# Optimization experiments

Hardware: AMD Instinct MI355X
Metric: run time of the kernel (lower is better)

Reference implementation:

```python
import jax, jax.numpy as jnp
import numpy as np

N = 4096
SPECIES = 100
FEA = 64        # atom_emb_dim
NBR_FEA = 64    # num gaussians
MAX_NBRS = 12
LN_EPS = 1e-5

# GaussianSmearing constants: linspace(0, 8, 64)
_OFFSET = jnp.linspace(0.0, 8.0, NBR_FEA)
_COEFF = -0.5 / float(8.0 / (NBR_FEA - 1)) ** 2


def _uniform(key, shape, fan_in):
    s = 1.0 / np.sqrt(fan_in)
    return jax.random.uniform(key, shape, minval=-s, maxval=s, dtype=jnp.float32)


def setup_inputs() -> dict:
    key = jax.random.key(0)
    ks = jax.random.split(key, 20)
    lat_pred = jnp.eye(3, dtype=jnp.float32) * 8.0 + 0.2 * jax.random.normal(ks[0], (3, 3), dtype=jnp.float32)
    fracs_pred = jax.random.uniform(ks[1], (N, 3), dtype=jnp.float32)
    species_logits = jax.random.normal(ks[2], (N, SPECIES), dtype=jnp.float32)
    occ_logits = jax.random.normal(ks[3], (N,), dtype=jnp.float32)
    # params
    emb_w = _uniform(ks[4], (SPECIES, FEA), SPECIES)
    emb_b = _uniform(ks[5], (FEA,), SPECIES)
    in1 = 2 * FEA + NBR_FEA  # 192
    w1 = _uniform(ks[6], (in1, 2 * FEA), in1)
    b1 = _uniform(ks[7], (2 * FEA,), in1)
    g1 = jnp.ones((2 * FEA,), jnp.float32)
    be1 = jnp.zeros((2 * FEA,), jnp.float32)
    w2 = _uniform(ks[8], (in1, 2 * FEA), in1)
    b2 = _uniform(ks[9], (2 * FEA,), in1)
    g2 = jnp.ones((2 * FEA,), jnp.float32)
    be2 = jnp.zeros((2 * FEA,), jnp.float32)
    fc_w = _uniform(ks[10], (FEA, 1), FEA)
    fc_b = _uniform(ks[11], (1,), FEA)
    return dict(lat_pred=lat_pred, fracs_pred=fracs_pred, species_logits=species_logits,
                occ_logits=occ_logits, emb_w=emb_w, emb_b=emb_b,
                w1=w1, b1=b1, g1=g1, be1=be1, w2=w2, b2=b2, g2=g2, be2=be2,
                fc_w=fc_w, fc_b=fc_b)


def _layernorm(x, g, b):
    m = jnp.mean(x, axis=-1, keepdims=True)
    v = jnp.var(x, axis=-1, keepdims=True)
    return (x - m) * jax.lax.rsqrt(v + LN_EPS) * g + b


def _cgcnn_layer(atom, nbr_atom, nbr_fea, w, b, g, be):
    # atom: [N,F]; nbr_atom: [N,M,F]; nbr_fea: [N,M,K]
    n, m = nbr_atom.shape[:2]
    atom_exp = jnp.broadcast_to(atom[:, None, :], (n, m, atom.shape[-1]))
    total = jnp.concatenate([atom_exp, nbr_atom, nbr_fea], axis=2)  # [N,M,2F+K]
    z = _layernorm(total @ w + b, g, be)                            # [N,M,2F]
    nbr_filter, nbr_core = jnp.split(z, 2, axis=2)
    nbr_sumed = jnp.sum(jax.nn.sigmoid(nbr_filter) * jax.nn.softplus(nbr_core), axis=1)
    return jax.nn.softplus(atom + nbr_sumed)


def reference(lat_pred, fracs_pred, species_logits, occ_logits,
              emb_w, emb_b, w1, b1, g1, be1, w2, b2, g2, be2, fc_w, fc_b):
    species_probs = jax.nn.softmax(species_logits, axis=-1)
    atom_fea = species_probs @ emb_w + emb_b                         # [N,F]
    diff = fracs_pred[:, None, :] - fracs_pred[None, :, :]           # [N,N,3]
    diff = diff - jnp.round(diff)                                    # min-image
    cart = diff @ lat_pred                                           # [N,N,3]
    dist = jnp.linalg.norm(cart, axis=-1)                            # [N,N]
    dist = dist + jnp.eye(dist.shape[0], dtype=dist.dtype) * 100.0
    k = min(MAX_NBRS, dist.shape[1] - 1)
    neg_d, nbr_idx = jax.lax.top_k(-dist, k)                         # smallest k
    nbr_dist = -neg_d                                                # [N,k]
    nbr_fea = jnp.exp(_COEFF * (nbr_dist[..., None] - _OFFSET) ** 2) # [N,k,K]
    nbr_atom_fea = atom_fea[nbr_idx]                                 # [N,k,F]
    atom_fea = _cgcnn_layer(atom_fea, nbr_atom_fea, nbr_fea, w1, b1, g1, be1)
    atom_fea = _cgcnn_layer(atom_fea, nbr_atom_fea, nbr_fea, w2, b2, g2, be2)
    occ_probs = jax.nn.sigmoid(occ_logits)[:, None]                  # [N,1]
    graph_fea = jnp.sum(atom_fea * occ_probs, axis=0) / (jnp.sum(occ_probs) + 1e-6)
    return graph_fea @ fc_w + fc_b                                   # [1]
```

## Files before the change

### kernel.cpp

```cpp
#include <hip/hip_runtime.h>
#include <math.h>

#define N_ATOMS 4096
#define SPECIES 100
#define FEA 64
#define M_NBR 12

typedef unsigned short u16;
typedef __attribute__((ext_vector_type(8))) _Float16 f16x8;
typedef __attribute__((ext_vector_type(4))) float f32x4;

constexpr float LN_EPS = 1e-5f;
constexpr float GAUSS_COEFF = -31.0078125f;
constexpr float D2_INF = 3.4e38f;

__device__ __forceinline__ float sigmoidf_(float x){
    return __fdividef(1.0f, 1.0f + __expf(-x));
}
__device__ __forceinline__ float softplusf_(float x){
    return fmaxf(x, 0.0f) + __logf(1.0f + __expf(-fabsf(x)));
}
__device__ __forceinline__ u16 f16bits(_Float16 h){ return *(u16*)&h; }

__global__ __launch_bounds__(256) void k_setup(const float* __restrict__ fracs,
        const float* __restrict__ w1, const float* __restrict__ w2,
        const float* __restrict__ logits, const float* __restrict__ emb_w,
        const float* __restrict__ emb_b,
        float* __restrict__ fx, float* __restrict__ fy, float* __restrict__ fz,
        u16* __restrict__ wpk, float* __restrict__ atom0, u16* __restrict__ a0f){
    __shared__ float sE[4][SPECIES];
    int b = blockIdx.x, t = threadIdx.x;
    if (b < 192){
        int gid = b * 256 + t;
        int layer = gid / 24576;
        int e = gid % 24576;
        int k = e >> 7, n = e & 127;
        float x = (layer ? w2 : w1)[e];
        int mat = layer * 3 + (k >> 6);
        int kk = k & 63;
        int ch = kk >> 5, lg2 = (kk >> 3) & 3, i = kk & 7;
        int nt = n >> 4, lr2 = n & 15;
        wpk[mat * 8192 + ((ch * 8 + nt) * 64 + (lg2 * 16 + lr2)) * 8 + i] = f16bits((_Float16)x);
    } else if (b < 208){
        int j = (b - 192) * 256 + t;
        fx[j] = fracs[j*3+0];
        fy[j] = fracs[j*3+1];
        fz[j] = fracs[j*3+2];
    } else {
        int grp = t >> 6, f = t & 63;
        int a = (b - 208) * 4 + grp;
        const float* lg = logits + (long)a * SPECIES;
        float l0 = lg[f];
        float l1 = (f + 64 < SPECIES) ? lg[f + 64] : -1e30f;
        float mx = fmaxf(l0, l1);
        #pragma unroll
        for (int off = 32; off; off >>= 1) mx = fmaxf(mx, __shfl_xor(mx, off));
        float e0 = __expf(l0 - mx);
        float e1 = (f + 64 < SPECIES) ? __expf(l1 - mx) : 0.0f;
        sE[grp][f] = e0;
        if (f + 64 < SPECIES) sE[grp][64 + f] = e1;
        float sm = e0 + e1;
        #pragma unroll
        for (int off = 32; off; off >>= 1) sm += __shfl_xor(sm, off);
        __syncthreads();
        float acc = 0.0f;
        for (int s = 0; s < SPECIES; ++s) acc += sE[grp][s] * emb_w[s * FEA + f];
        float v = acc / sm + emb_b[f];
        atom0[(long)a * FEA + f] = v;
        a0f[a * FEA + f] = f16bits((_Float16)v);
    }
}

__global__ __launch_bounds__(256) void k_topk(const float* __restrict__ fx,
        const float* __restrict__ fy, const float* __restrict__ fz,
        const float* __restrict__ lat, int* __restrict__ nbr_idx,
        float* __restrict__ nbr_dist){
    __shared__ int   hist[256];
    __shared__ int   cnt;
    __shared__ float sThr;
    __shared__ float candD[256];
    __shared__ int   candI[256];
    int i = blockIdx.x, tid = threadIdx.x;
    hist[tid] = 0;
    if (tid == 0) cnt = 0;
    __syncthreads();
    float l00=lat[0],l01=lat[1],l02=lat[2];
    float l10=lat[3],l11=lat[4],l12=lat[5];
    float l20=lat[6],l21=lat[7],l22=lat[8];
    float xi = fx[i], yi = fy[i], zi = fz[i];
    float d2r[16];
    #pragma unroll
    for (int k = 0; k < 16; ++k){
        int j = tid + k * 256;
        float dx = xi - fx[j];
        float dy = yi - fy[j];
        float dz = zi - fz[j];
        dx -= rintf(dx); dy -= rintf(dy); dz -= rintf(dz);
        float cx = dx*l00 + dy*l10 + dz*l20;
        float cy = dx*l01 + dy*l11 + dz*l21;
        float cz = dx*l02 + dy*l12 + dz*l22;
        float d2 = cx*cx + cy*cy + cz*cz;
        if (j == i) d2 = D2_INF;
        d2r[k] = d2;
        if (d2 < 4.0f) atomicAdd(&hist[(int)(d2 * 64.0f)], 1);
    }
    __syncthreads();
    if (tid < 64){
        int s0 = hist[4*tid] + hist[4*tid+1] + hist[4*tid+2] + hist[4*tid+3];
        int sc = s0;
        #pragma unroll
        for (int off = 1; off < 64; off <<= 1){
            int o = __shfl_up(sc, off);
            if (tid >= off) sc += o;
        }
        unsigned long long mball = __ballot(sc >= M_NBR);
        if (mball == 0ULL){
            if (tid == 0) sThr = 1e30f;
        } else {
            int gbin = __ffsll(mball) - 1;
            if (tid == gbin){
                int c = sc - s0;
                float th = 4.0f;
                #pragma unroll
                for (int b = 0; b < 4; ++b){
                    c += hist[4*gbin + b];
                    if (c >= M_NBR){ th = (float)(4*gbin + b + 1) * (1.0f/64.0f); break; }
                }
                sThr = th;
            }
        }
    }
    __syncthreads();
    float thr = sThr;
    #pragma unroll
    for (int k = 0; k < 16; ++k){
        if (d2r[k] < thr){
            int p = atomicAdd(&cnt, 1);
            if (p < 256){ candD[p] = d2r[k]; candI[p] = tid + k * 256; }
        }
    }
    __syncthreads();
    int n = cnt < 256 ? cnt : 256;
    for (int c = tid; c < n; c += 256){
        float dv = candD[c]; int iv = candI[c];
        int rank = 0;
        for (int s = 0; s < n; ++s){
            float ds_ = candD[s]; int is_ = candI[s];
            rank += (ds_ < dv || (ds_ == dv && is_ < iv)) ? 1 : 0;
        }
        if (rank < M_NBR){
            nbr_idx[i * M_NBR + rank]  = iv;
            nbr_dist[i * M_NBR + rank] = sqrtf(dv);
        }
    }
}

__global__ __launch_bounds__(192) void k_fused(
        const float* __restrict__ atom0F, const u16* __restrict__ a0f,
        const int* __restrict__ nbr_idx, const float* __restrict__ nbr_dist,
        const u16* __restrict__ wpk,
        const float* __restrict__ b1, const float* __restrict__ g1, const float* __restrict__ be1,
        const float* __restrict__ b2, const float* __restrict__ g2, const float* __restrict__ be2,
        float* __restrict__ outF)
{
    __shared__ float sS1[4][132];
    __shared__ float prod[48][68];
    __shared__ float sSF[4][64];
    __shared__ u16   sSH[4][64];
    __shared__ float sS2[4][132];

    const int t = threadIdx.x;
    const int w = t >> 6, l = t & 63;
    const int lg = l >> 4, lr = l & 15;
    const int blk = blockIdx.x;
    const int row = blk * 48 + w * 16 + lr;

    const int nid = nbr_idx[row];
    f16x8 nfr[2];
    nfr[0] = *(const f16x8*)(a0f + nid * 64 + lg * 8);
    nfr[1] = *(const f16x8*)(a0f + nid * 64 + 32 + lg * 8);

    f16x8 saf[2];
    if (w == 1){
        #pragma unroll
        for (int c = 0; c < 2; ++c)
            saf[c] = (lr < 4) ? *(const f16x8*)(a0f + (blk * 4 + lr) * 64 + c * 32 + lg * 8)
                              : (f16x8)0;
    }

    float g1v[8], be1v[8], g2v[8], be2v[8];
    #pragma unroll
    for (int nt = 0; nt < 8; ++nt){
        int c = nt * 16 + lr;
        g1v[nt] = g1[c]; be1v[nt] = be1[c];
        g2v[nt] = g2[c]; be2v[nt] = be2[c];
    }

    const float dist = nbr_dist[row];
    f16x8 ga[2];
    #pragma unroll
    for (int c = 0; c < 2; ++c)
        #pragma unroll
        for (int i = 0; i < 8; ++i){
            int k = c * 32 + lg * 8 + i;
            float dd = dist - (float)k * (8.0f / 63.0f);
            ga[c][i] = (_Float16)__expf(GAUSS_COEFF * dd * dd);
        }

    int aloc[4];
    #pragma unroll
    for (int rr = 0; rr < 4; ++rr)
        aloc[rr] = (w * 16 + lg * 4 + rr) / 12;

    const u16* ws1 = wpk;
    const u16* wn1 = wpk + 1 * 8192;
    const u16* wg1 = wpk + 2 * 8192;
    const u16* ws2 = wpk + 3 * 8192;
    const u16* wn2 = wpk + 4 * 8192;
    const u16* wg2 = wpk + 5 * 8192;

    if (w == 1){
        f32x4 a1[8];
        #pragma unroll
        for (int nt = 0; nt < 8; ++nt) a1[nt] = 0.0f;
        #pragma unroll
        for (int c = 0; c < 2; ++c)
            #pragma unroll
            for (int nt = 0; nt < 8; ++nt){
                const f16x8 b = *(const f16x8*)(ws1 + ((c * 8 + nt) * 64 + l) * 8);
                a1[nt] = __builtin_amdgcn_mfma_f32_16x16x32_f16(saf[c], b, a1[nt], 0, 0, 0);
            }
        if (lg == 0){
            #pragma unroll
            for (int nt = 0; nt < 8; ++nt)
                #pragma unroll
                for (int rr = 0; rr < 4; ++rr)
                    sS1[rr][nt * 16 + lr] = a1[nt][rr] + b1[nt * 16 + lr];
        }
    }

    f32x4 acc[8], acc2[8];
    #pragma unroll
    for (int nt = 0; nt < 8; ++nt){ acc[nt] = 0.0f; acc2[nt] = 0.0f; }
    #pragma unroll
    for (int c = 0; c < 2; ++c)
        #pragma unroll
        for (int nt = 0; nt < 8; ++nt){
            const f16x8 bn1 = *(const f16x8*)(wn1 + ((c * 8 + nt) * 64 + l) * 8);
            acc[nt]  = __builtin_amdgcn_mfma_f32_16x16x32_f16(nfr[c], bn1, acc[nt], 0, 0, 0);
            const f16x8 bg1 = *(const f16x8*)(wg1 + ((c * 8 + nt) * 64 + l) * 8);
            acc[nt]  = __builtin_amdgcn_mfma_f32_16x16x32_f16(ga[c],  bg1, acc[nt], 0, 0, 0);
            const f16x8 bn2 = *(const f16x8*)(wn2 + ((c * 8 + nt) * 64 + l) * 8);
            acc2[nt] = __builtin_amdgcn_mfma_f32_16x16x32_f16(nfr[c], bn2, acc2[nt], 0, 0, 0);
            const f16x8 bg2 = *(const f16x8*)(wg2 + ((c * 8 + nt) * 64 + l) * 8);
            acc2[nt] = __builtin_amdgcn_mfma_f32_16x16x32_f16(ga[c],  bg2, acc2[nt], 0, 0, 0);
        }
    __syncthreads();

    {
        float s[4] = {0,0,0,0}, q[4] = {0,0,0,0};
        #pragma unroll
        for (int nt = 0; nt < 8; ++nt)
            #pragma unroll
            for (int rr = 0; rr < 4; ++rr){
                float v = acc[nt][rr] + sS1[aloc[rr]][nt * 16 + lr];
                acc[nt][rr] = v;
                s[rr] += v; q[rr] += v * v;
            }
        #pragma unroll
        for (int rr = 0; rr < 4; ++rr){
            #pragma unroll
            for (int m = 1; m < 16; m <<= 1){
                s[rr] += __shfl_xor(s[rr], m);
                q[rr] += __shfl_xor(q[rr], m);
            }
        }
        #pragma unroll
        for (int rr = 0; rr < 4; ++rr){
            float mean = s[rr] * (1.0f / 128.0f);
            float var  = q[rr] * (1.0f / 128.0f) - mean * mean;
            float inv  = rsqrtf(var + LN_EPS);
            #pragma unroll
            for (int nt = 0; nt < 4; ++nt){
                float zf = (acc[nt][rr]     - mean) * inv * g1v[nt]     + be1v[nt];
                float zc = (acc[nt + 4][rr] - mean) * inv * g1v[nt + 4] + be1v[nt + 4];
                prod[w * 16 + lg * 4 + rr][nt * 16 + lr] = sigmoidf_(zf) * softplusf_(zc);
            }
        }
    }
    __syncthreads();

    #pragma unroll
    for (int rep = 0; rep < 2; ++rep){
        int item = t + rep * 192;
        if (item < 256){
            int a_ = item >> 6, c = item & 63;
            float sm = 0.0f;
            #pragma unroll
            for (int m = 0; m < 12; ++m) sm += prod[a_ * 12 + m][c];
            float o = softplusf_(atom0F[(long)(blk * 4 + a_) * 64 + c] + sm);
            sSF[a_][c] = o;
            sSH[a_][c] = f16bits((_Float16)o);
        }
    }
    __syncthreads();

    if (w == 0){
        f16x8 af[2];
        #pragma unroll
        for (int c = 0; c < 2; ++c)
            af[c] = (lr < 4) ? *(const f16x8*)(&sSH[lr][c * 32 + lg * 8]) : (f16x8)0;
        f32x4 a2[8];
        #pragma unroll
        for (int nt = 0; nt < 8; ++nt) a2[nt] = 0.0f;
        #pragma unroll
        for (int c = 0; c < 2; ++c)
            #pragma unroll
            for (int nt = 0; nt < 8; ++nt){
                const f16x8 b = *(const f16x8*)(ws2 + ((c * 8 + nt) * 64 + l) * 8);
                a2[nt] = __builtin_amdgcn_mfma_f32_16x16x32_f16(af[c], b, a2[nt], 0, 0, 0);
            }
        if (lg == 0){
            #pragma unroll
            for (int nt = 0; nt < 8; ++nt)
                #pragma unroll
                for (int rr = 0; rr < 4; ++rr)
                    sS2[rr][nt * 16 + lr] = a2[nt][rr] + b2[nt * 16 + lr];
        }
    }
    __syncthreads();

    {
        float s[4] = {0,0,0,0}, q[4] = {0,0,0,0};
        #pragma unroll
        for (int nt = 0; nt < 8; ++nt)
            #pragma unroll
            for (int rr = 0; rr < 4; ++rr){
                float v = acc2[nt][rr] + sS2[aloc[rr]][nt * 16 + lr];
                acc2[nt][rr] = v;
                s[rr] += v; q[rr] += v * v;
            }
        #pragma unroll
        for (int rr = 0; rr < 4; ++rr){
            #pragma unroll
            for (int m = 1; m < 16; m <<= 1){
                s[rr] += __shfl_xor(s[rr], m);
                q[rr] += __shfl_xor(q[rr], m);
            }
        }
        #pragma unroll
        for (int rr = 0; rr < 4; ++rr){
            float mean = s[rr] * (1.0f / 128.0f);
            float var  = q[rr] * (1.0f / 128.0f) - mean * mean;
            float inv  = rsqrtf(var + LN_EPS);
            #pragma unroll
            for (int nt = 0; nt < 4; ++nt){
                float zf = (acc2[nt][rr]     - mean) * inv * g2v[nt]     + be2v[nt];
                float zc = (acc2[nt + 4][rr] - mean) * inv * g2v[nt + 4] + be2v[nt + 4];
                prod[w * 16 + lg * 4 + rr][nt * 16 + lr] = sigmoidf_(zf) * softplusf_(zc);
            }
        }
    }
    __syncthreads();

    #pragma unroll
    for (int rep = 0; rep < 2; ++rep){
        int item = t + rep * 192;
        if (item < 256){
            int a_ = item >> 6, c = item & 63;
            float sm = 0.0f;
            #pragma unroll
            for (int m = 0; m < 12; ++m) sm += prod[a_ * 12 + m][c];
            outF[(long)(blk * 4 + a_) * 64 + c] = softplusf_(sSF[a_][c] + sm);
        }
    }
}

__global__ __launch_bounds__(256) void k_partial(const float* __restrict__ atom,
        const float* __restrict__ occ, float* __restrict__ partials){
    int b = blockIdx.x, tid = threadIdx.x;
    int f = tid & 63, sub = tid >> 6;
    __shared__ float sAcc[256];
    float acc = 0.0f;
    for (int it = 0; it < 16; ++it){
        int a = b * 64 + sub + it * 4;
        float p = sigmoidf_(occ[a]);
        acc += atom[(long)a * FEA + f] * p;
    }
    sAcc[tid] = acc;
    __syncthreads();
    if (tid < 64){
        float s = sAcc[f] + sAcc[64 + f] + sAcc[128 + f] + sAcc[192 + f];
        partials[b * 65 + f] = s;
        float po = sigmoidf_(occ[b * 64 + f]);
        #pragma unroll
        for (int off = 32; off; off >>= 1) po += __shfl_down(po, off);
        if (f == 0) partials[b * 65 + 64] = po;
    }
}

__global__ __launch_bounds__(64) void k_final(const float* __restrict__ partials,
        const float* __restrict__ fc_w, const float* __restrict__ fc_b,
        float* __restrict__ out){
    int f = threadIdx.x;
    float num = 0.0f;
    for (int p = 0; p < 64; ++p) num += partials[p * 65 + f];
    float occs = partials[f * 65 + 64];
    #pragma unroll
    for (int off = 32; off; off >>= 1) occs += __shfl_down(occs, off);
    occs = __shfl(occs, 0);
    float gf = num / (occs + 1e-6f);
    float v = gf * fc_w[f];
    #pragma unroll
    for (int off = 32; off; off >>= 1) v += __shfl_down(v, off);
    if (f == 0) out[0] = v + fc_b[0];
}

extern "C" void kernel_launch(void* const* d_in, const int* in_sizes, int n_in,
                              void* d_out, int out_size, void* d_ws, size_t ws_size,
                              hipStream_t stream) {
    const float* lat    = (const float*)d_in[0];
    const float* fracs  = (const float*)d_in[1];
    const float* slog   = (const float*)d_in[2];
    const float* occ    = (const float*)d_in[3];
    const float* emb_w  = (const float*)d_in[4];
    const float* emb_b  = (const float*)d_in[5];
    const float* w1     = (const float*)d_in[6];
    const float* b1     = (const float*)d_in[7];
    const float* g1     = (const float*)d_in[8];
    const float* be1    = (const float*)d_in[9];
    const float* w2     = (const float*)d_in[10];
    const float* b2     = (const float*)d_in[11];
    const float* g2     = (const float*)d_in[12];
    const float* be2    = (const float*)d_in[13];
    const float* fc_w   = (const float*)d_in[14];
    const float* fc_b   = (const float*)d_in[15];
    float* out = (float*)d_out;

    char* ws = (char*)d_ws;
    auto alloc = [&](size_t bytes) -> void* {
        void* p = (void*)ws;
        ws += (bytes + 255) & ~(size_t)255;
        return p;
    };
    int*   nbr_idx  = (int*)  alloc((size_t)N_ATOMS * M_NBR * 4);
    float* nbr_dist = (float*)alloc((size_t)N_ATOMS * M_NBR * 4);
    float* atom0    = (float*)alloc((size_t)N_ATOMS * FEA * 4);
    float* atom1    = (float*)alloc((size_t)N_ATOMS * FEA * 4);
    u16*   a0f      = (u16*)  alloc((size_t)N_ATOMS * FEA * 2);
    u16*   wpk      = (u16*)  alloc((size_t)6 * 8192 * 2);
    float* fxa      = (float*)alloc((size_t)N_ATOMS * 4);
    float* fya      = (float*)alloc((size_t)N_ATOMS * 4);
    float* fza      = (float*)alloc((size_t)N_ATOMS * 4);
    float* partials = (float*)alloc((size_t)64 * 65 * 4);

    k_setup  <<<208 + N_ATOMS / 4, 256, 0, stream>>>(fracs, w1, w2, slog, emb_w, emb_b,
                fxa, fya, fza, wpk, atom0, a0f);
    k_topk   <<<N_ATOMS, 256, 0, stream>>>(fxa, fya, fza, lat, nbr_idx, nbr_dist);
    k_fused  <<<N_ATOMS / 4, 192, 0, stream>>>(atom0, a0f, nbr_idx, nbr_dist,
                wpk, b1, g1, be1, b2, g2, be2, atom1);
    k_partial<<<64, 256, 0, stream>>>(atom1, occ, partials);
    k_final  <<<1, 64, 0, stream>>>(partials, fc_w, fc_b, out);
}
```

Before: 62.11 us.

## Compute self-projection redundantly per wave to drop block barriers and defer layer-2 GEMM

Every wave now computes the self-atom projection into its own shared-memory slot instead of one wave doing it for all, which removes two block-wide barriers. The layer-2 neighbour GEMM is moved after layer 1 so the acc2 registers are not live during layer 1, lowering register pressure. Residual atom features are prefetched early, and the aggregation loops are flattened. In exchange the small self-projection MFMAs run three times redundantly and shared memory grows.

Result: no change. 62.13 us (+0.0%).

```diff
diff --git a/kernel.cpp b/kernel.cpp
--- a/kernel.cpp
+++ b/kernel.cpp
@@ -163,11 +163,11 @@
         const float* __restrict__ b2, const float* __restrict__ g2, const float* __restrict__ be2,
         float* __restrict__ outF)
 {
-    __shared__ float sS1[4][132];
+    __shared__ float sS1w[3][4][132];
+    __shared__ float sS2w[3][4][132];
     __shared__ float prod[48][68];
     __shared__ float sSF[4][64];
     __shared__ u16   sSH[4][64];
-    __shared__ float sS2[4][132];
 
     const int t = threadIdx.x;
     const int w = t >> 6, l = t & 63;
@@ -181,19 +181,20 @@
     nfr[1] = *(const f16x8*)(a0f + nid * 64 + 32 + lg * 8);
 
     f16x8 saf[2];
-    if (w == 1){
-        #pragma unroll
-        for (int c = 0; c < 2; ++c)
-            saf[c] = (lr < 4) ? *(const f16x8*)(a0f + (blk * 4 + lr) * 64 + c * 32 + lg * 8)
-                              : (f16x8)0;
-    }
-
-    float g1v[8], be1v[8], g2v[8], be2v[8];
+    #pragma unroll
+    for (int c = 0; c < 2; ++c)
+        saf[c] = (lr < 4) ? *(const f16x8*)(a0f + (blk * 4 + lr) * 64 + c * 32 + lg * 8)
+                          : (f16x8)0;
+
+    const float* a0flat = atom0F + (long)blk * 256;
+    float res0 = a0flat[t];
+    float res1 = (t < 64) ? a0flat[192 + t] : 0.0f;
+
+    float g1v[8], be1v[8];
     #pragma unroll
     for (int nt = 0; nt < 8; ++nt){
         int c = nt * 16 + lr;
         g1v[nt] = g1[c]; be1v[nt] = be1[c];
-        g2v[nt] = g2[c]; be2v[nt] = be2[c];
     }
 
     const float dist = nbr_dist[row];
@@ -219,7 +220,7 @@
     const u16* wn2 = wpk + 4 * 8192;
     const u16* wg2 = wpk + 5 * 8192;
 
-    if (w == 1){
+    {
         f32x4 a1[8];
         #pragma unroll
         for (int nt = 0; nt < 8; ++nt) a1[nt] = 0.0f;
@@ -235,27 +236,22 @@
             for (int nt = 0; nt < 8; ++nt)
                 #pragma unroll
                 for (int rr = 0; rr < 4; ++rr)
-                    sS1[rr][nt * 16 + lr] = a1[nt][rr] + b1[nt * 16 + lr];
-        }
-    }
-
-    f32x4 acc[8], acc2[8];
-    #pragma unroll
-    for (int nt = 0; nt < 8; ++nt){ acc[nt] = 0.0f; acc2[nt] = 0.0f; }
+                    sS1w[w][rr][nt * 16 + lr] = a1[nt][rr] + b1[nt * 16 + lr];
+        }
+    }
+
+    f32x4 acc[8];
+    #pragma unroll
+    for (int nt = 0; nt < 8; ++nt) acc[nt] = 0.0f;
     #pragma unroll
     for (int c = 0; c < 2; ++c)
         #pragma unroll
         for (int nt = 0; nt < 8; ++nt){
-            const f16x8 bn1 = *(const f16x8*)(wn1 + ((c * 8 + nt) * 64 + l) * 8);
-            acc[nt]  = __builtin_amdgcn_mfma_f32_16x16x32_f16(nfr[c], bn1, acc[nt], 0, 0, 0);
-            const f16x8 bg1 = *(const f16x8*)(wg1 + ((c * 8 + nt) * 64 + l) * 8);
-            acc[nt]  = __builtin_amdgcn_mfma_f32_16x16x32_f16(ga[c],  bg1, acc[nt], 0, 0, 0);
-            const f16x8 bn2 = *(const f16x8*)(wn2 + ((c * 8 + nt) * 64 + l) * 8);
-            acc2[nt] = __builtin_amdgcn_mfma_f32_16x16x32_f16(nfr[c], bn2, acc2[nt], 0, 0, 0);
-            const f16x8 bg2 = *(const f16x8*)(wg2 + ((c * 8 + nt) * 64 + l) * 8);
-            acc2[nt] = __builtin_amdgcn_mfma_f32_16x16x32_f16(ga[c],  bg2, acc2[nt], 0, 0, 0);
-        }
-    __syncthreads();
+            const f16x8 bn = *(const f16x8*)(wn1 + ((c * 8 + nt) * 64 + l) * 8);
+            acc[nt] = __builtin_amdgcn_mfma_f32_16x16x32_f16(nfr[c], bn, acc[nt], 0, 0, 0);
+            const f16x8 bg = *(const f16x8*)(wg1 + ((c * 8 + nt) * 64 + l) * 8);
+            acc[nt] = __builtin_amdgcn_mfma_f32_16x16x32_f16(ga[c], bg, acc[nt], 0, 0, 0);
+        }
 
     {
         float s[4] = {0,0,0,0}, q[4] = {0,0,0,0};
@@ -263,7 +259,7 @@
         for (int nt = 0; nt < 8; ++nt)
             #pragma unroll
             for (int rr = 0; rr < 4; ++rr){
-                float v = acc[nt][rr] + sS1[aloc[rr]][nt * 16 + lr];
+                float v = acc[nt][rr] + sS1w[w][aloc[rr]][nt * 16 + lr];
                 acc[nt][rr] = v;
                 s[rr] += v; q[rr] += v * v;
             }
@@ -290,22 +286,33 @@
     }
     __syncthreads();
 
-    #pragma unroll
-    for (int rep = 0; rep < 2; ++rep){
-        int item = t + rep * 192;
-        if (item < 256){
-            int a_ = item >> 6, c = item & 63;
-            float sm = 0.0f;
-            #pragma unroll
-            for (int m = 0; m < 12; ++m) sm += prod[a_ * 12 + m][c];
-            float o = softplusf_(atom0F[(long)(blk * 4 + a_) * 64 + c] + sm);
-            sSF[a_][c] = o;
-            sSH[a_][c] = f16bits((_Float16)o);
-        }
-    }
-    __syncthreads();
-
-    if (w == 0){
+    {
+        int a_ = t >> 6, c = t & 63;
+        float sm = 0.0f;
+        #pragma unroll
+        for (int m = 0; m < 12; ++m) sm += prod[a_ * 12 + m][c];
+        float o = softplusf_(res0 + sm);
+        sSF[a_][c] = o;
+        sSH[a_][c] = f16bits((_Float16)o);
+        if (t < 64){
+            float sm2 = 0.0f;
+            #pragma unroll
+            for (int m = 0; m < 12; ++m) sm2 += prod[36 + m][c];
+            float o2 = softplusf_(res1 + sm2);
+            sSF[3][c] = o2;
+            sSH[3][c] = f16bits((_Float16)o2);
+        }
+    }
+    __syncthreads();
+
+    float g2v[8], be2v[8];
+    #pragma unroll
+    for (int nt = 0; nt < 8; ++nt){
+        int c = nt * 16 + lr;
+        g2v[nt] = g2[c]; be2v[nt] = be2[c];
+    }
+
+    {
         f16x8 af[2];
         #pragma unroll
         for (int c = 0; c < 2; ++c)
@@ -325,10 +332,22 @@
             for (int nt = 0; nt < 8; ++nt)
                 #pragma unroll
                 for (int rr = 0; rr < 4; ++rr)
-                    sS2[rr][nt * 16 + lr] = a2[nt][rr] + b2[nt * 16 + lr];
-        }
-    }
-    __syncthreads();
+                    sS2w[w][rr][nt * 16 + lr] = a2[nt][rr] + b2[nt * 16 + lr];
+        }
+    }
+
+    f32x4 acc2[8];
+    #pragma unroll
+    for (int nt = 0; nt < 8; ++nt) acc2[nt] = 0.0f;
+    #pragma unroll
+    for (int c = 0; c < 2; ++c)
+        #pragma unroll
+        for (int nt = 0; nt < 8; ++nt){
+            const f16x8 bn = *(const f16x8*)(wn2 + ((c * 8 + nt) * 64 + l) * 8);
+            acc2[nt] = __builtin_amdgcn_mfma_f32_16x16x32_f16(nfr[c], bn, acc2[nt], 0, 0, 0);
+            const f16x8 bg = *(const f16x8*)(wg2 + ((c * 8 + nt) * 64 + l) * 8);
+            acc2[nt] = __builtin_amdgcn_mfma_f32_16x16x32_f16(ga[c], bg, acc2[nt], 0, 0, 0);
+        }
 
     {
         float s[4] = {0,0,0,0}, q[4] = {0,0,0,0};
@@ -336,7 +355,7 @@
         for (int nt = 0; nt < 8; ++nt)
             #pragma unroll
             for (int rr = 0; rr < 4; ++rr){
-                float v = acc2[nt][rr] + sS2[aloc[rr]][nt * 16 + lr];
+                float v = acc2[nt][rr] + sS2w[w][aloc[rr]][nt * 16 + lr];
                 acc2[nt][rr] = v;
                 s[rr] += v; q[rr] += v * v;
             }
@@ -363,15 +382,17 @@
     }
     __syncthreads();
 
-    #pragma unroll
-    for (int rep = 0; rep < 2; ++rep){
-        int item = t + rep * 192;
-        if (item < 256){
-            int a_ = item >> 6, c = item & 63;
-            float sm = 0.0f;
-            #pragma unroll
-            for (int m = 0; m < 12; ++m) sm += prod[a_ * 12 + m][c];
-            outF[(long)(blk * 4 + a_) * 64 + c] = softplusf_(sSF[a_][c] + sm);
+    {
+        int a_ = t >> 6, c = t & 63;
+        float sm = 0.0f;
+        #pragma unroll
+        for (int m = 0; m < 12; ++m) sm += prod[a_ * 12 + m][c];
+        outF[(long)blk * 256 + t] = softplusf_(sSF[a_][c] + sm);
+        if (t < 64){
+            float sm2 = 0.0f;
+            #pragma unroll
+            for (int m = 0; m < 12; ++m) sm2 += prod[36 + m][c];
+            outF[(long)blk * 256 + 192 + t] = softplusf_(sSF[3][c] + sm2);
         }
     }
 }
```

## Restructure fused CGCNN kernel to one wavefront per atom

Applied to the files above, without the earlier changes.

Replaces the 3-wave, 4-atoms-per-block fused layer kernel with a single-wavefront kernel that handles one atom per block. The 12 neighbours are padded to 16 MFMA rows, the self-feature GEMM is folded into the same MFMA accumulation, and the neighbour sum is done with lane shuffles instead of shared-memory reductions. The goal is to drop most block barriers and shared-memory traffic and to launch 4096 small blocks for better latency hiding. In exchange, every block redundantly runs the self GEMM over 16 rows, 4 padded rows are wasted per tile, and each block reloads the full weight set, which raises L2 traffic.

After: 61.85 us. About the same (-0.4%).

```diff
diff --git a/kernel.cpp b/kernel.cpp
--- a/kernel.cpp
+++ b/kernel.cpp
@@ -155,7 +155,7 @@
     }
 }
 
-__global__ __launch_bounds__(192) void k_fused(
+__global__ __launch_bounds__(64, 4) void k_atom(
         const float* __restrict__ atom0F, const u16* __restrict__ a0f,
         const int* __restrict__ nbr_idx, const float* __restrict__ nbr_dist,
         const u16* __restrict__ wpk,
@@ -163,40 +163,26 @@
         const float* __restrict__ b2, const float* __restrict__ g2, const float* __restrict__ be2,
         float* __restrict__ outF)
 {
-    __shared__ float sS1[4][132];
-    __shared__ float prod[48][68];
-    __shared__ float sSF[4][64];
-    __shared__ u16   sSH[4][64];
-    __shared__ float sS2[4][132];
-
-    const int t = threadIdx.x;
-    const int w = t >> 6, l = t & 63;
+    __shared__ u16   sH[64];
+    __shared__ float sO[64];
+
+    const int a = blockIdx.x;
+    const int l = threadIdx.x;
     const int lg = l >> 4, lr = l & 15;
-    const int blk = blockIdx.x;
-    const int row = blk * 48 + w * 16 + lr;
-
-    const int nid = nbr_idx[row];
-    f16x8 nfr[2];
+
+    const int slot = (lr < 12) ? lr : 11;
+    const int nid  = nbr_idx[a * M_NBR + slot];
+    const float dist = nbr_dist[a * M_NBR + slot];
+    f16x8 nfr[2], saf[2];
     nfr[0] = *(const f16x8*)(a0f + nid * 64 + lg * 8);
     nfr[1] = *(const f16x8*)(a0f + nid * 64 + 32 + lg * 8);
-
-    f16x8 saf[2];
-    if (w == 1){
-        #pragma unroll
-        for (int c = 0; c < 2; ++c)
-            saf[c] = (lr < 4) ? *(const f16x8*)(a0f + (blk * 4 + lr) * 64 + c * 32 + lg * 8)
-                              : (f16x8)0;
-    }
-
-    float g1v[8], be1v[8], g2v[8], be2v[8];
-    #pragma unroll
-    for (int nt = 0; nt < 8; ++nt){
-        int c = nt * 16 + lr;
-        g1v[nt] = g1[c]; be1v[nt] = be1[c];
-        g2v[nt] = g2[c]; be2v[nt] = be2[c];
-    }
-
-    const float dist = nbr_dist[row];
+    saf[0] = *(const f16x8*)(a0f + a * 64 + lg * 8);
+    saf[1] = *(const f16x8*)(a0f + a * 64 + 32 + lg * 8);
+    float resv[4];
+    #pragma unroll
+    for (int nt = 0; nt < 4; ++nt)
+        resv[nt] = atom0F[(long)a * 64 + nt * 16 + lr];
+
     f16x8 ga[2];
     #pragma unroll
     for (int c = 0; c < 2; ++c)
@@ -207,66 +193,39 @@
             ga[c][i] = (_Float16)__expf(GAUSS_COEFF * dd * dd);
         }
 
-    int aloc[4];
-    #pragma unroll
-    for (int rr = 0; rr < 4; ++rr)
-        aloc[rr] = (w * 16 + lg * 4 + rr) / 12;
-
-    const u16* ws1 = wpk;
-    const u16* wn1 = wpk + 1 * 8192;
-    const u16* wg1 = wpk + 2 * 8192;
-    const u16* ws2 = wpk + 3 * 8192;
-    const u16* wn2 = wpk + 4 * 8192;
-    const u16* wg2 = wpk + 5 * 8192;
-
-    if (w == 1){
-        f32x4 a1[8];
-        #pragma unroll
-        for (int nt = 0; nt < 8; ++nt) a1[nt] = 0.0f;
+    #pragma unroll 1
+    for (int layer = 0; layer < 2; ++layer){
+        const u16* wb = wpk + layer * 3 * 8192;
+        const float* bb  = layer ? b2  : b1;
+        const float* gg  = layer ? g2  : g1;
+        const float* bee = layer ? be2 : be1;
+
+        f32x4 acc[8];
+        #pragma unroll
+        for (int nt = 0; nt < 8; ++nt) acc[nt] = 0.0f;
         #pragma unroll
         for (int c = 0; c < 2; ++c)
             #pragma unroll
             for (int nt = 0; nt < 8; ++nt){
-                const f16x8 b = *(const f16x8*)(ws1 + ((c * 8 + nt) * 64 + l) * 8);
-                a1[nt] = __builtin_amdgcn_mfma_f32_16x16x32_f16(saf[c], b, a1[nt], 0, 0, 0);
-            }
-        if (lg == 0){
-            #pragma unroll
-            for (int nt = 0; nt < 8; ++nt)
-                #pragma unroll
-                for (int rr = 0; rr < 4; ++rr)
-                    sS1[rr][nt * 16 + lr] = a1[nt][rr] + b1[nt * 16 + lr];
-        }
-    }
-
-    f32x4 acc[8], acc2[8];
-    #pragma unroll
-    for (int nt = 0; nt < 8; ++nt){ acc[nt] = 0.0f; acc2[nt] = 0.0f; }
-    #pragma unroll
-    for (int c = 0; c < 2; ++c)
+                const f16x8 bS = *(const f16x8*)(wb +          ((c * 8 + nt) * 64 + l) * 8);
+                const f16x8 bN = *(const f16x8*)(wb +  8192 + ((c * 8 + nt) * 64 + l) * 8);
+                const f16x8 bG = *(const f16x8*)(wb + 16384 + ((c * 8 + nt) * 64 + l) * 8);
+                acc[nt] = __builtin_amdgcn_mfma_f32_16x16x32_f16(saf[c], bS, acc[nt], 0, 0, 0);
+                acc[nt] = __builtin_amdgcn_mfma_f32_16x16x32_f16(nfr[c], bN, acc[nt], 0, 0, 0);
+                acc[nt] = __builtin_amdgcn_mfma_f32_16x16x32_f16(ga[c],  bG, acc[nt], 0, 0, 0);
+            }
+
+        float s[4] = {0,0,0,0}, q[4] = {0,0,0,0};
         #pragma unroll
         for (int nt = 0; nt < 8; ++nt){
-            const f16x8 bn1 = *(const f16x8*)(wn1 + ((c * 8 + nt) * 64 + l) * 8);
-            acc[nt]  = __builtin_amdgcn_mfma_f32_16x16x32_f16(nfr[c], bn1, acc[nt], 0, 0, 0);
-            const f16x8 bg1 = *(const f16x8*)(wg1 + ((c * 8 + nt) * 64 + l) * 8);
-            acc[nt]  = __builtin_amdgcn_mfma_f32_16x16x32_f16(ga[c],  bg1, acc[nt], 0, 0, 0);
-            const f16x8 bn2 = *(const f16x8*)(wn2 + ((c * 8 + nt) * 64 + l) * 8);
-            acc2[nt] = __builtin_amdgcn_mfma_f32_16x16x32_f16(nfr[c], bn2, acc2[nt], 0, 0, 0);
-            const f16x8 bg2 = *(const f16x8*)(wg2 + ((c * 8 + nt) * 64 + l) * 8);
-            acc2[nt] = __builtin_amdgcn_mfma_f32_16x16x32_f16(ga[c],  bg2, acc2[nt], 0, 0, 0);
-        }
-    __syncthreads();
-
-    {
-        float s[4] = {0,0,0,0}, q[4] = {0,0,0,0};
-        #pragma unroll
-        for (int nt = 0; nt < 8; ++nt)
+            float bv = bb[nt * 16 + lr];
             #pragma unroll
             for (int rr = 0; rr < 4; ++rr){
-                float v = acc[nt][rr] + sS1[aloc[rr]][nt * 16 + lr];
+                float v = acc[nt][rr] + bv;
                 acc[nt][rr] = v;
                 s[rr] += v; q[rr] += v * v;
             }
+        }
         #pragma unroll
         for (int rr = 0; rr < 4; ++rr){
             #pragma unroll
@@ -275,103 +234,47 @@
                 q[rr] += __shfl_xor(q[rr], m);
             }
         }
-        #pragma unroll
-        for (int rr = 0; rr < 4; ++rr){
-            float mean = s[rr] * (1.0f / 128.0f);
-            float var  = q[rr] * (1.0f / 128.0f) - mean * mean;
-            float inv  = rsqrtf(var + LN_EPS);
-            #pragma unroll
-            for (int nt = 0; nt < 4; ++nt){
-                float zf = (acc[nt][rr]     - mean) * inv * g1v[nt]     + be1v[nt];
-                float zc = (acc[nt + 4][rr] - mean) * inv * g1v[nt + 4] + be1v[nt + 4];
-                prod[w * 16 + lg * 4 + rr][nt * 16 + lr] = sigmoidf_(zf) * softplusf_(zc);
-            }
-        }
-    }
-    __syncthreads();
-
-    #pragma unroll
-    for (int rep = 0; rep < 2; ++rep){
-        int item = t + rep * 192;
-        if (item < 256){
-            int a_ = item >> 6, c = item & 63;
-            float sm = 0.0f;
-            #pragma unroll
-            for (int m = 0; m < 12; ++m) sm += prod[a_ * 12 + m][c];
-            float o = softplusf_(atom0F[(long)(blk * 4 + a_) * 64 + c] + sm);
-            sSF[a_][c] = o;
-            sSH[a_][c] = f16bits((_Float16)o);
-        }
-    }
-    __syncthreads();
-
-    if (w == 0){
-        f16x8 af[2];
-        #pragma unroll
-        for (int c = 0; c < 2; ++c)
-            af[c] = (lr < 4) ? *(const f16x8*)(&sSH[lr][c * 32 + lg * 8]) : (f16x8)0;
-        f32x4 a2[8];
-        #pragma unroll
-        for (int nt = 0; nt < 8; ++nt) a2[nt] = 0.0f;
-        #pragma unroll
-        for (int c = 0; c < 2; ++c)
-            #pragma unroll
-            for (int nt = 0; nt < 8; ++nt){
-                const f16x8 b = *(const f16x8*)(ws2 + ((c * 8 + nt) * 64 + l) * 8);
-                a2[nt] = __builtin_amdgcn_mfma_f32_16x16x32_f16(af[c], b, a2[nt], 0, 0, 0);
-            }
-        if (lg == 0){
-            #pragma unroll
-            for (int nt = 0; nt < 8; ++nt)
-                #pragma unroll
-                for (int rr = 0; rr < 4; ++rr)
-                    sS2[rr][nt * 16 + lr] = a2[nt][rr] + b2[nt * 16 + lr];
-        }
-    }
-    __syncthreads();
-
-    {
-        float s[4] = {0,0,0,0}, q[4] = {0,0,0,0};
-        #pragma unroll
-        for (int nt = 0; nt < 8; ++nt)
+        float nsum[4];
+        #pragma unroll
+        for (int nt = 0; nt < 4; ++nt){
+            float gf = gg[nt * 16 + lr],      bef = bee[nt * 16 + lr];
+            float gc = gg[64 + nt * 16 + lr], bec = bee[64 + nt * 16 + lr];
+            float part = 0.0f;
             #pragma unroll
             for (int rr = 0; rr < 4; ++rr){
-                float v = acc2[nt][rr] + sS2[aloc[rr]][nt * 16 + lr];
-                acc2[nt][rr] = v;
-                s[rr] += v; q[rr] += v * v;
-            }
-        #pragma unroll
-        for (int rr = 0; rr < 4; ++rr){
-            #pragma unroll
-            for (int m = 1; m < 16; m <<= 1){
-                s[rr] += __shfl_xor(s[rr], m);
-                q[rr] += __shfl_xor(q[rr], m);
-            }
-        }
-        #pragma unroll
-        for (int rr = 0; rr < 4; ++rr){
-            float mean = s[rr] * (1.0f / 128.0f);
-            float var  = q[rr] * (1.0f / 128.0f) - mean * mean;
-            float inv  = rsqrtf(var + LN_EPS);
-            #pragma unroll
-            for (int nt = 0; nt < 4; ++nt){
-                float zf = (acc2[nt][rr]     - mean) * inv * g2v[nt]     + be2v[nt];
-                float zc = (acc2[nt + 4][rr] - mean) * inv * g2v[nt + 4] + be2v[nt + 4];
-                prod[w * 16 + lg * 4 + rr][nt * 16 + lr] = sigmoidf_(zf) * softplusf_(zc);
-            }
-        }
-    }
-    __syncthreads();
-
-    #pragma unroll
-    for (int rep = 0; rep < 2; ++rep){
-        int item = t + rep * 192;
-        if (item < 256){
-            int a_ = item >> 6, c = item & 63;
-            float sm = 0.0f;
-            #pragma unroll
-            for (int m = 0; m < 12; ++m) sm += prod[a_ * 12 + m][c];
-            outF[(long)(blk * 4 + a_) * 64 + c] = softplusf_(sSF[a_][c] + sm);
+                float mean = s[rr] * (1.0f / 128.0f);
+                float var  = q[rr] * (1.0f / 128.0f) - mean * mean;
+                float inv  = rsqrtf(var + LN_EPS);
+                float zf = (acc[nt][rr]     - mean) * inv * gf + bef;
+                float zc = (acc[nt + 4][rr] - mean) * inv * gc + bec;
+                part += sigmoidf_(zf) * softplusf_(zc);
+            }
+            if (lg == 3) part = 0.0f;
+            part += __shfl_xor(part, 16);
+            part += __shfl_xor(part, 32);
+            nsum[nt] = part;
+        }
+        #pragma unroll
+        for (int nt = 0; nt < 4; ++nt)
+            resv[nt] = softplusf_(resv[nt] + nsum[nt]);
+
+        if (layer == 0){
+            if (lg == 0){
+                #pragma unroll
+                for (int nt = 0; nt < 4; ++nt)
+                    sH[nt * 16 + lr] = f16bits((_Float16)resv[nt]);
+            }
+            __syncthreads();
+            saf[0] = *(const f16x8*)(&sH[lg * 8]);
+            saf[1] = *(const f16x8*)(&sH[32 + lg * 8]);
+        } else {
+            if (lg == 0){
+                #pragma unroll
+                for (int nt = 0; nt < 4; ++nt)
+                    sO[nt * 16 + lr] = resv[nt];
+            }
+            __syncthreads();
+            outF[(long)a * 64 + l] = sO[l];
         }
     }
 }
@@ -457,7 +360,7 @@
     k_setup  <<<208 + N_ATOMS / 4, 256, 0, stream>>>(fracs, w1, w2, slog, emb_w, emb_b,
                 fxa, fya, fza, wpk, atom0, a0f);
     k_topk   <<<N_ATOMS, 256, 0, stream>>>(fxa, fya, fza, lat, nbr_idx, nbr_dist);
-    k_fused  <<<N_ATOMS / 4, 192, 0, stream>>>(atom0, a0f, nbr_idx, nbr_dist,
+    k_atom   <<<N_ATOMS, 64, 0, stream>>>(atom0, a0f, nbr_idx, nbr_dist,
                 wpk, b1, g1, be1, b2, g2, be2, atom1);
     k_partial<<<64, 256, 0, stream>>>(atom1, occ, partials);
     k_final  <<<1, 64, 0, stream>>>(partials, fc_w, fc_b, out);
```
